# Performance work log

Hardware: AMD Instinct MI355X
Metric: run time of the kernel (lower is better)

## Reference

```python
import jax, jax.numpy as jnp
import numpy as np

B, D_IN, D_H, D_OUT, D_INT = 1024, 2048, 4096, 2048, 1024


def fwht(x):
    """Fast Walsh-Hadamard transform over a length-2^k vector (unnormalized),
    faithful to the torch chunk/cat butterfly loop."""
    n = x.shape[0]
    k = int(n).bit_length() - 1
    for i in range(k):
        y = x.reshape(2 ** i, 2, -1)        # split butterfly level i
        x = jnp.stack([y[:, 0] + y[:, 1], y[:, 0] - y[:, 1]], axis=1)
    return x.reshape(n)


def fastfood(V, BB, Pi, GG, DD):
    """fastfood_torched: pad -> B*x -> H -> permute -> G* -> H -> slice/scale."""
    LL = BB.shape[0]
    vpad = jnp.zeros((LL,), V.dtype).at[: V.shape[0]].set(V)
    m5 = fwht(fwht(BB * vpad)[Pi] * GG)
    divisor = jnp.sqrt(LL * jnp.sum(GG * GG))
    return m5[:DD] / (divisor * np.sqrt(float(DD) / LL))


def _ff_vars(key, DD):
    LL = 1 << int(np.ceil(np.log2(DD)))
    k1, k2, k3 = jax.random.split(key, 3)
    BB = jnp.where(jax.random.uniform(k1, (LL,)) < 0.5, -1.0, 1.0).astype(jnp.float32)
    Pi = jax.random.permutation(k2, LL).astype(jnp.int32)
    GG = jax.random.normal(k3, (LL,), dtype=jnp.float32)
    return BB, Pi, GG


def setup_inputs():
    key = jax.random.key(0)
    ks = jax.random.split(key, 8)
    x = jax.random.normal(ks[0], (B, D_IN), dtype=jnp.float32)
    V = jax.random.normal(ks[1], (D_INT,), dtype=jnp.float32) * 0.01
    W1_0 = jax.random.normal(ks[2], (D_H, D_IN), dtype=jnp.float32) * 0.02
    b1_0 = jnp.zeros((D_H,), jnp.float32)
    W2_0 = jax.random.normal(ks[3], (D_OUT, D_H), dtype=jnp.float32) * 0.02
    b2_0 = jnp.zeros((D_OUT,), jnp.float32)
    BB_W1, Pi_W1, GG_W1 = _ff_vars(ks[4], D_H * D_IN)
    BB_b1, Pi_b1, GG_b1 = _ff_vars(ks[5], D_H)
    BB_W2, Pi_W2, GG_W2 = _ff_vars(ks[6], D_OUT * D_H)
    BB_b2, Pi_b2, GG_b2 = _ff_vars(ks[7], D_OUT)
    return dict(x=x, V=V, W1_0=W1_0, b1_0=b1_0, W2_0=W2_0, b2_0=b2_0,
                BB_W1=BB_W1, Pi_W1=Pi_W1, GG_W1=GG_W1,
                BB_b1=BB_b1, Pi_b1=Pi_b1, GG_b1=GG_b1,
                BB_W2=BB_W2, Pi_W2=Pi_W2, GG_W2=GG_W2,
                BB_b2=BB_b2, Pi_b2=Pi_b2, GG_b2=GG_b2)


def reference(x, V, W1_0, b1_0, W2_0, b2_0,
              BB_W1, Pi_W1, GG_W1, BB_b1, Pi_b1, GG_b1,
              BB_W2, Pi_W2, GG_W2, BB_b2, Pi_b2, GG_b2):
    # Reconstruct each parameter: theta = theta0 + fastfood(V).view(shape)
    W1 = W1_0 + fastfood(V, BB_W1, Pi_W1, GG_W1, D_H * D_IN).reshape(D_H, D_IN)
    b1 = b1_0 + fastfood(V, BB_b1, Pi_b1, GG_b1, D_H)
    W2 = W2_0 + fastfood(V, BB_W2, Pi_W2, GG_W2, D_OUT * D_H).reshape(D_OUT, D_H)
    b2 = b2_0 + fastfood(V, BB_b2, Pi_b2, GG_b2, D_OUT)
    # Wrapped module forward (2-layer MLP)
    h = jax.nn.relu(x @ W1.T + b1)
    return h @ W2.T + b2
```

## Files before the change

### kernel.cpp

```cpp
#include <hip/hip_runtime.h>
#include <hip/hip_bf16.h>
#include <stdint.h>


typedef __attribute__((ext_vector_type(8))) short bf16x8;
typedef __attribute__((ext_vector_type(8))) short short8;
typedef __attribute__((ext_vector_type(4))) float f32x4;

__device__ __forceinline__ ushort f2bf(float f) {
  union { float f; uint32_t u; } v; v.f = f;
  return (ushort)((v.u + 0x7FFFu + ((v.u >> 16) & 1u)) >> 16);
}
__device__ __forceinline__ float bf2f(ushort u) {
  union { uint32_t u; float f; } v; v.u = (uint32_t)u << 16; return v.f;
}

__device__ __forceinline__ void gload_lds16(const void* g, void* l) {
  __builtin_amdgcn_global_load_lds(
      (const __attribute__((address_space(1))) void*)g,
      (__attribute__((address_space(3))) void*)l, 16, 0, 0);
}

__device__ __forceinline__ void wait_vm0()  { asm volatile("s_waitcnt vmcnt(0)"  ::: "memory"); }
__device__ __forceinline__ void wait_lgkm0(){ asm volatile("s_waitcnt lgkmcnt(0)" ::: "memory"); }
__device__ __forceinline__ void barrier_raw(){ asm volatile("s_barrier" ::: "memory"); }
__device__ __forceinline__ void lds_barrier() {
  wait_lgkm0();
  barrier_raw();
  __builtin_amdgcn_sched_barrier(0);
}

template <int NN>
__device__ __forceinline__ void wht_inreg(float* v) {
#pragma unroll
  for (int h = 1; h < NN; h <<= 1)
#pragma unroll
    for (int g = 0; g < NN; g += (h << 1))
#pragma unroll
      for (int k = 0; k < h; ++k) {
        float a = v[g + k], b = v[g + k + h];
        v[g + k] = a + b; v[g + k + h] = a - b;
      }
}

__global__ __launch_bounds__(256) void prep(
    const float4* __restrict__ x4, ushort4* __restrict__ xb4,
    const float* __restrict__ V,
    const float* __restrict__ BBW1, const float* __restrict__ BBW2,
    float* __restrict__ t1, float* __restrict__ t2,
    const float* __restrict__ BBb1, const int* __restrict__ Pib1,
    const float* __restrict__ GGb1, const float* __restrict__ b10,
    const float* __restrict__ BBb2, const int* __restrict__ Pib2,
    const float* __restrict__ GGb2, const float* __restrict__ b20,
    float* __restrict__ ob1, float* __restrict__ ob2) {
  __shared__ float ts[1024];
  __shared__ float zs[4096];
  __shared__ float red[4];
  const int bid = blockIdx.x;
  const int tid = threadIdx.x;

  if (bid < 2048) {
    int i = bid * 256 + tid;
    float4 v = x4[i];
    ushort4 o;
    o.x = f2bf(v.x); o.y = f2bf(v.y); o.z = f2bf(v.z); o.w = f2bf(v.w);
    xb4[i] = o;
    return;
  }

  if (bid < 2050) {
    const int which = bid - 2048;
    const float* BB = which ? BBW2 : BBW1;
    float* t = which ? t2 : t1;
    for (int i = tid; i < 1024; i += 256) ts[i] = BB[i] * V[i];
    for (int st = 0; st < 10; ++st) {
      int half = 1 << st;
      __syncthreads();
      for (int j = tid; j < 512; j += 256) {
        int p = ((j >> st) << (st + 1)) | (j & (half - 1));
        float a = ts[p], b = ts[p + half];
        ts[p] = a + b; ts[p + half] = a - b;
      }
    }
    __syncthreads();
    for (int i = tid; i < 1024; i += 256) t[i] = ts[i];
    return;
  }

  {
    const int which = bid - 2050;
    const int L = which ? 2048 : 4096;
    const float* BB = which ? BBb2 : BBb1;
    const int* Pi = which ? Pib2 : Pib1;
    const float* GG = which ? GGb2 : GGb1;
    const float* b0 = which ? b20 : b10;
    float* ob = which ? ob2 : ob1;

    for (int i = tid; i < 1024; i += 256) ts[i] = BB[i] * V[i];
    for (int st = 0; st < 10; ++st) {
      int half = 1 << st;
      __syncthreads();
      for (int j = tid; j < 512; j += 256) {
        int p = ((j >> st) << (st + 1)) | (j & (half - 1));
        float a = ts[p], b = ts[p + half];
        ts[p] = a + b; ts[p + half] = a - b;
      }
    }
    __syncthreads();
    float gsum = 0.f;
    for (int i = tid; i < L; i += 256) {
      int pi = Pi[i];
      float g = GG[i];
      gsum += g * g;
      zs[i] = ts[pi & 1023] * g;
    }
    for (int o = 32; o > 0; o >>= 1) gsum += __shfl_down(gsum, o);
    if ((tid & 63) == 0) red[tid >> 6] = gsum;
    __syncthreads();
    float ssum = red[0] + red[1] + red[2] + red[3];
    for (int st = 0; (1 << st) < L; ++st) {
      int half = 1 << st;
      __syncthreads();
      for (int j = tid; j < (L >> 1); j += 256) {
        int p = ((j >> st) << (st + 1)) | (j & (half - 1));
        float a = zs[p], b = zs[p + half];
        zs[p] = a + b; zs[p + half] = a - b;
      }
    }
    __syncthreads();
    float scale = rsqrtf((float)L * ssum);
    for (int i = tid; i < L; i += 256) ob[i] = b0[i] + zs[i] * scale;
  }
}

__global__ __launch_bounds__(256) void ff_pass1(
    const int* __restrict__ Pi1, const float* __restrict__ GG1,
    const int* __restrict__ Pi2, const float* __restrict__ GG2,
    const float* __restrict__ t1, const float* __restrict__ t2,
    ushort* __restrict__ inter1, ushort* __restrict__ inter2,
    float* __restrict__ partials) {
  __shared__ float ts[1024];
  __shared__ float zs[8448];
  __shared__ float red[4];
  int tid = threadIdx.x;
  int wsel = blockIdx.x >> 10;
  int blk = blockIdx.x & 1023;
  const int* Pi = wsel ? Pi2 : Pi1;
  const float* GG = wsel ? GG2 : GG1;
  const float* t = wsel ? t2 : t1;
  ushort* inter = wsel ? inter2 : inter1;
  size_t base = (size_t)blk * 8192;

  for (int i = tid; i < 1024; i += 256) ts[i] = t[i];
  __syncthreads();

  const int4* Pi4 = (const int4*)(Pi + base);
  const float4* GG4 = (const float4*)(GG + base);
  float gsum = 0.f;
#pragma unroll
  for (int q = 0; q < 8; ++q) {
    int u = (q << 8) + tid;
    int4 p4 = Pi4[u];
    float4 g4 = GG4[u];
    gsum += g4.x * g4.x + g4.y * g4.y + g4.z * g4.z + g4.w * g4.w;
    int i0 = u << 2;
    float4 z;
    z.x = ts[p4.x & 1023] * g4.x;
    z.y = ts[p4.y & 1023] * g4.y;
    z.z = ts[p4.z & 1023] * g4.z;
    z.w = ts[p4.w & 1023] * g4.w;
    *(float4*)&zs[i0 + (i0 >> 5)] = z;
  }
  for (int o = 32; o > 0; o >>= 1) gsum += __shfl_down(gsum, o);
  if ((tid & 63) == 0) red[tid >> 6] = gsum;
  __syncthreads();
  if (tid == 0) partials[blockIdx.x] = red[0] + red[1] + red[2] + red[3];

  float v[32];
  {
    int o = (tid & 7) | ((tid >> 3) << 8);
#pragma unroll
    for (int r = 0; r < 32; ++r) { int i = o + (r << 3); v[r] = zs[i + (i >> 5)]; }
    wht_inreg<32>(v);
#pragma unroll
    for (int r = 0; r < 32; ++r) { int i = o + (r << 3); zs[i + (i >> 5)] = v[r]; }
  }
  __syncthreads();
  {
#pragma unroll
    for (int r = 0; r < 32; ++r) { int i = tid | (r << 8); v[r] = zs[i + (i >> 5)]; }
    wht_inreg<32>(v);
#pragma unroll
    for (int r = 0; r < 32; ++r) { int i = tid | (r << 8); zs[i + (i >> 5)] = v[r]; }
  }
  __syncthreads();
  {
    int tp = ((tid & 63) << 3) | ((tid >> 6) << 11);
#pragma unroll
    for (int j = 0; j < 4; ++j)
#pragma unroll
      for (int k = 0; k < 8; ++k) { int i = tp + (j << 9) + k; v[(j << 3) + k] = zs[i + (i >> 5)]; }
#pragma unroll
    for (int j = 0; j < 4; ++j) wht_inreg<8>(v + (j << 3));
#pragma unroll
    for (int j = 0; j < 4; ++j) {
      short8 s;
#pragma unroll
      for (int k = 0; k < 8; ++k) s[k] = (short)f2bf(v[(j << 3) + k]);
      *(short8*)(inter + base + tp + (j << 9)) = s;
    }
  }
}

__global__ __launch_bounds__(512) void ff_pass2(
    const ushort* __restrict__ inter1, const ushort* __restrict__ inter2,
    const float* __restrict__ W01, const float* __restrict__ W02,
    const float* __restrict__ partials,
    ushort* __restrict__ W1b, ushort* __restrict__ W2b) {
  __shared__ ushort tile[65536];
  __shared__ float red[8];
  const int tid = threadIdx.x;
  const int wsel = blockIdx.x >> 7;
  const int cb = (blockIdx.x & 127) << 6;
  const ushort* __restrict__ inter = wsel ? inter2 : inter1;
  const float* __restrict__ W0 = wsel ? W02 : W01;
  ushort* __restrict__ Wb = wsel ? W2b : W1b;
  char* tb = (char*)tile;

  float s = partials[(wsel << 10) + tid] + partials[(wsel << 10) + tid + 512];
  for (int o = 32; o > 0; o >>= 1) s += __shfl_down(s, o);
  if ((tid & 63) == 0) red[tid >> 6] = s;

#pragma unroll
  for (int h = 0; h < 2; ++h) {
    int r = tid + (h << 9);
    const ushort* gp = inter + ((size_t)r << 13) + cb;
#pragma unroll
    for (int j = 0; j < 8; ++j) {
      short8 d = *(const short8*)(gp + (j << 3));
      *(short8*)(tb + (r << 7) + ((j ^ (r & 7)) << 4)) = d;
    }
  }
  float4 w0a0[8], w0b0[8];
  {
    const size_t gb = ((size_t)tid << 13) + cb;
#pragma unroll
    for (int j = 0; j < 8; ++j) {
      w0a0[j] = *(const float4*)(W0 + gb + (j << 3));
      w0b0[j] = *(const float4*)(W0 + gb + (j << 3) + 4);
    }
  }
  lds_barrier();
  float ssum = 0.f;
#pragma unroll
  for (int k = 0; k < 8; ++k) ssum += red[k];
  const float sc = rsqrtf(8388608.f * ssum);

  const int p = tid & 31;
  const int j0 = p >> 2;
  const int ob = (p & 3) << 2;
#pragma unroll
  for (int swp = 0; swp < 2; ++swp) {
    const int ge = (tid >> 5) + (swp << 4);
    float va[32], vb[32];
#pragma unroll
    for (int r = 0; r < 32; ++r) {
      int row = (ge << 5) + r;
      ushort2 u = *(const ushort2*)(tb + (row << 7) + ((j0 ^ (row & 7)) << 4) + ob);
      va[r] = bf2f(u.x); vb[r] = bf2f(u.y);
    }
    wht_inreg<32>(va); wht_inreg<32>(vb);
#pragma unroll
    for (int r = 0; r < 32; ++r) {
      int row = (ge << 5) + r;
      ushort2 u; u.x = f2bf(va[r]); u.y = f2bf(vb[r]);
      *(ushort2*)(tb + (row << 7) + ((j0 ^ (row & 7)) << 4) + ob) = u;
    }
  }
  lds_barrier();
#pragma unroll
  for (int swp = 0; swp < 2; ++swp) {
    const int ge = (tid >> 5) + (swp << 4);
    float va[32], vb[32];
#pragma unroll
    for (int r = 0; r < 32; ++r) {
      int row = ge + (r << 5);
      ushort2 u = *(const ushort2*)(tb + (row << 7) + ((j0 ^ (row & 7)) << 4) + ob);
      va[r] = bf2f(u.x); vb[r] = bf2f(u.y);
    }
    wht_inreg<32>(va); wht_inreg<32>(vb);
#pragma unroll
    for (int r = 0; r < 32; ++r) {
      int row = ge + (r << 5);
      ushort2 u; u.x = f2bf(va[r]); u.y = f2bf(vb[r]);
      *(ushort2*)(tb + (row << 7) + ((j0 ^ (row & 7)) << 4) + ob) = u;
    }
  }
  float4 w0a1[8], w0b1[8];
  {
    const size_t gb = ((size_t)(tid + 512) << 13) + cb;
#pragma unroll
    for (int j = 0; j < 8; ++j) {
      w0a1[j] = *(const float4*)(W0 + gb + (j << 3));
      w0b1[j] = *(const float4*)(W0 + gb + (j << 3) + 4);
    }
  }
  lds_barrier();
  {
    const int r = tid;
    const size_t gb = ((size_t)r << 13) + cb;
#pragma unroll
    for (int j = 0; j < 8; ++j) {
      short8 d = *(const short8*)(tb + (r << 7) + ((j ^ (r & 7)) << 4));
      short8 o;
      o[0] = (short)f2bf(bf2f((ushort)d[0]) * sc + w0a0[j].x);
      o[1] = (short)f2bf(bf2f((ushort)d[1]) * sc + w0a0[j].y);
      o[2] = (short)f2bf(bf2f((ushort)d[2]) * sc + w0a0[j].z);
      o[3] = (short)f2bf(bf2f((ushort)d[3]) * sc + w0a0[j].w);
      o[4] = (short)f2bf(bf2f((ushort)d[4]) * sc + w0b0[j].x);
      o[5] = (short)f2bf(bf2f((ushort)d[5]) * sc + w0b0[j].y);
      o[6] = (short)f2bf(bf2f((ushort)d[6]) * sc + w0b0[j].z);
      o[7] = (short)f2bf(bf2f((ushort)d[7]) * sc + w0b0[j].w);
      *(short8*)(Wb + gb + (j << 3)) = o;
    }
  }
  {
    const int r = tid + 512;
    const size_t gb = ((size_t)r << 13) + cb;
#pragma unroll
    for (int j = 0; j < 8; ++j) {
      short8 d = *(const short8*)(tb + (r << 7) + ((j ^ (r & 7)) << 4));
      short8 o;
      o[0] = (short)f2bf(bf2f((ushort)d[0]) * sc + w0a1[j].x);
      o[1] = (short)f2bf(bf2f((ushort)d[1]) * sc + w0a1[j].y);
      o[2] = (short)f2bf(bf2f((ushort)d[2]) * sc + w0a1[j].z);
      o[3] = (short)f2bf(bf2f((ushort)d[3]) * sc + w0a1[j].w);
      o[4] = (short)f2bf(bf2f((ushort)d[4]) * sc + w0b1[j].x);
      o[5] = (short)f2bf(bf2f((ushort)d[5]) * sc + w0b1[j].y);
      o[6] = (short)f2bf(bf2f((ushort)d[6]) * sc + w0b1[j].z);
      o[7] = (short)f2bf(bf2f((ushort)d[7]) * sc + w0b1[j].w);
      *(short8*)(Wb + gb + (j << 3)) = o;
    }
  }
}

template <int NT>
__global__ __launch_bounds__(256) void gemm_sp(
    const ushort* __restrict__ A, const ushort* __restrict__ B,
    ushort* __restrict__ P0, ushort* __restrict__ P1,
    ushort* __restrict__ P2, ushort* __restrict__ P3,
    int M, int N, int K) {
  __shared__ ushort As[2][8192];
  __shared__ ushort Bs[2][8192];
  const int tid = threadIdx.x;
  const int w = tid >> 6, l = tid & 63;
  const int wr = w >> 1, wc = w & 1;
  const int brow = blockIdx.y << 7, bcol = blockIdx.x << 7;
  const int lrow = l >> 3;
  const int csrc = ((l & 7) ^ lrow) << 3;
  const int l15 = l & 15;
  const int x7 = l15 & 7;
  const int z = blockIdx.z;
  const int kb = z * (NT << 6);
  ushort* __restrict__ P = z == 0 ? P0 : z == 1 ? P1 : z == 2 ? P2 : P3;
  f32x4 acc[4][4] = {};

  const ushort* pa = A + (size_t)(brow + (w << 5) + lrow) * K + kb + csrc;
  const ushort* pb = B + (size_t)(bcol + (w << 5) + lrow) * K + kb + csrc;
  const size_t K8 = (size_t)K << 3;

#define STAGE(buf, tt)                                                      \
  {                                                                         \
    const ushort* qa = pa + ((tt) << 6);                                    \
    const ushort* qb = pb + ((tt) << 6);                                    \
    _Pragma("unroll")                                                       \
    for (int i = 0; i < 4; ++i) {                                           \
      gload_lds16(qa + K8 * i, &As[buf][(((w << 2) + i) << 9)]);            \
      gload_lds16(qb + K8 * i, &Bs[buf][(((w << 2) + i) << 9)]);            \
    }                                                                       \
  }

  STAGE(0, 0);
  for (int t = 0; t < NT; ++t) {
    wait_vm0();
    barrier_raw();
    if (t + 1 < NT) STAGE((t + 1) & 1, t + 1);
    const ushort* Acur = As[t & 1];
    const ushort* Bcur = Bs[t & 1];
    bf16x8 af[2][4], bfr[2][4];
#pragma unroll
    for (int kk = 0; kk < 2; ++kk) {
      int c8 = (kk << 2) + (l >> 4);
#pragma unroll
      for (int m = 0; m < 4; ++m)
        af[kk][m] = *(const bf16x8*)&Acur[(((wr << 6) + (m << 4) + l15) << 6) + ((c8 ^ x7) << 3)];
#pragma unroll
      for (int n = 0; n < 4; ++n)
        bfr[kk][n] = *(const bf16x8*)&Bcur[(((wc << 6) + (n << 4) + l15) << 6) + ((c8 ^ x7) << 3)];
    }
    wait_lgkm0();
#pragma unroll
    for (int kk = 0; kk < 2; ++kk)
#pragma unroll
      for (int m = 0; m < 4; ++m)
#pragma unroll
        for (int n = 0; n < 4; ++n)
          acc[m][n] = __builtin_amdgcn_mfma_f32_16x16x32_bf16(af[kk][m], bfr[kk][n], acc[m][n], 0, 0, 0);
  }
#undef STAGE

#pragma unroll
  for (int n = 0; n < 4; ++n) {
    int col = bcol + (wc << 6) + (n << 4) + l15;
#pragma unroll
    for (int m = 0; m < 4; ++m) {
      int row0 = brow + (wr << 6) + (m << 4) + ((l >> 4) << 2);
#pragma unroll
      for (int j = 0; j < 4; ++j)
        P[(size_t)(row0 + j) * N + col] = f2bf(acc[m][n][j]);
    }
  }
}

__global__ __launch_bounds__(256) void hfuse(
    const ushort4* __restrict__ G0, const ushort4* __restrict__ G1,
    const float* __restrict__ b1, ushort4* __restrict__ hb) {
  int i = blockIdx.x * 256 + threadIdx.x;
  ushort4 a = G0[i], b = G1[i];
  const float4 bv = *(const float4*)(b1 + ((i & 1023) << 2));
  ushort4 o;
  o.x = f2bf(fmaxf(bf2f(a.x) + bf2f(b.x) + bv.x, 0.f));
  o.y = f2bf(fmaxf(bf2f(a.y) + bf2f(b.y) + bv.y, 0.f));
  o.z = f2bf(fmaxf(bf2f(a.z) + bf2f(b.z) + bv.z, 0.f));
  o.w = f2bf(fmaxf(bf2f(a.w) + bf2f(b.w) + bv.w, 0.f));
  hb[i] = o;
}

__global__ __launch_bounds__(256) void reduce_out4(
    const ushort4* __restrict__ Q0, const ushort4* __restrict__ Q1,
    const ushort4* __restrict__ Q2, const ushort4* __restrict__ Q3,
    const float* __restrict__ b2, float4* __restrict__ out) {
  int i = blockIdx.x * 256 + threadIdx.x;
  ushort4 a = Q0[i], b = Q1[i], c = Q2[i], d = Q3[i];
  const float4 bb = *(const float4*)(b2 + ((i & 511) << 2));
  float4 o;
  o.x = bf2f(a.x) + bf2f(b.x) + bf2f(c.x) + bf2f(d.x) + bb.x;
  o.y = bf2f(a.y) + bf2f(b.y) + bf2f(c.y) + bf2f(d.y) + bb.y;
  o.z = bf2f(a.z) + bf2f(b.z) + bf2f(c.z) + bf2f(d.z) + bb.z;
  o.w = bf2f(a.w) + bf2f(b.w) + bf2f(c.w) + bf2f(d.w) + bb.w;
  out[i] = o;
}

extern "C" void kernel_launch(void* const* d_in, const int* in_sizes, int n_in,
                              void* d_out, int out_size, void* d_ws, size_t ws_size,
                              hipStream_t stream) {
  const float* x     = (const float*)d_in[0];
  const float* V     = (const float*)d_in[1];
  const float* W1_0  = (const float*)d_in[2];
  const float* b1_0  = (const float*)d_in[3];
  const float* W2_0  = (const float*)d_in[4];
  const float* b2_0  = (const float*)d_in[5];
  const float* BB_W1 = (const float*)d_in[6];
  const int*   Pi_W1 = (const int*)d_in[7];
  const float* GG_W1 = (const float*)d_in[8];
  const float* BB_b1 = (const float*)d_in[9];
  const int*   Pi_b1 = (const int*)d_in[10];
  const float* GG_b1 = (const float*)d_in[11];
  const float* BB_W2 = (const float*)d_in[12];
  const int*   Pi_W2 = (const int*)d_in[13];
  const float* GG_W2 = (const float*)d_in[14];
  const float* BB_b2 = (const float*)d_in[15];
  const int*   Pi_b2 = (const int*)d_in[16];
  const float* GG_b2 = (const float*)d_in[17];
  float* out = (float*)d_out;

  const size_t MB = 1048576ull;
  char* ws = (char*)d_ws;
  ushort* inter1 = (ushort*)(ws);
  ushort* G0     = (ushort*)(ws);
  ushort* G1     = (ushort*)(ws + 8 * MB);
  ushort* inter2 = (ushort*)(ws + 16 * MB);
  ushort* Q0     = (ushort*)(ws + 16 * MB);
  ushort* Q1     = (ushort*)(ws + 20 * MB);
  ushort* Q2     = (ushort*)(ws + 24 * MB);
  ushort* Q3     = (ushort*)(ws + 28 * MB);
  ushort* W1b    = (ushort*)(ws + 32 * MB);
  ushort* W2b    = (ushort*)(ws + 48 * MB);
  ushort* xb     = (ushort*)(ws + 64 * MB);
  ushort* hb     = (ushort*)(ws + 68 * MB);
  char*   S      = ws + 76 * MB;
  float*  t1     = (float*)(S);
  float*  t2     = (float*)(S + 4096);
  float*  b1     = (float*)(S + 8192);
  float*  b2     = (float*)(S + 8192 + 16384);
  float*  parts  = (float*)(S + 8192 + 16384 + 8192);

  prep<<<2052, 256, 0, stream>>>((const float4*)x, (ushort4*)xb, V,
                                 BB_W1, BB_W2, t1, t2,
                                 BB_b1, Pi_b1, GG_b1, b1_0,
                                 BB_b2, Pi_b2, GG_b2, b2_0, b1, b2);

  ff_pass1<<<2048, 256, 0, stream>>>(Pi_W1, GG_W1, Pi_W2, GG_W2, t1, t2,
                                     inter1, inter2, parts);
  ff_pass2<<<256, 512, 0, stream>>>(inter1, inter2, W1_0, W2_0, parts, W1b, W2b);

  gemm_sp<16><<<dim3(32, 8, 2), 256, 0, stream>>>(xb, W1b, G0, G1, nullptr, nullptr,
                                                  1024, 4096, 2048);
  hfuse<<<4096, 256, 0, stream>>>((const ushort4*)G0, (const ushort4*)G1, b1,
                                  (ushort4*)hb);
  gemm_sp<16><<<dim3(16, 8, 4), 256, 0, stream>>>(hb, W2b, Q0, Q1, Q2, Q3,
                                                  1024, 2048, 4096);
  reduce_out4<<<2048, 256, 0, stream>>>((const ushort4*)Q0, (const ushort4*)Q1,
                                        (const ushort4*)Q2, (const ushort4*)Q3,
                                        b2, (float4*)out);
}
```

Baseline: 155.5 us.

## Use 4-stage K=32 LDS pipeline in split-K GEMM instead of double buffering

The split-K bf16 GEMM now stages K tiles of 32 instead of 64 and keeps four LDS buffers, issuing three tiles ahead. It waits with partial vmcnt counts so later loads stay in flight. The swizzle and staging layout are reworked for 32-wide rows, and NT doubles to keep the same K per split. This aims to hide global load latency better, at the cost of twice as many barriers per K and less MFMA work between them.

Result: slower. 161.5 us (+3.9%).

```diff
diff --git a/kernel.cpp b/kernel.cpp
--- a/kernel.cpp
+++ b/kernel.cpp
@@ -21,6 +21,8 @@
       (__attribute__((address_space(3))) void*)l, 16, 0, 0);
 }
 
+__device__ __forceinline__ void wait_vm8()  { asm volatile("s_waitcnt vmcnt(8)"  ::: "memory"); }
+__device__ __forceinline__ void wait_vm4()  { asm volatile("s_waitcnt vmcnt(4)"  ::: "memory"); }
 __device__ __forceinline__ void wait_vm0()  { asm volatile("s_waitcnt vmcnt(0)"  ::: "memory"); }
 __device__ __forceinline__ void wait_lgkm0(){ asm volatile("s_waitcnt lgkmcnt(0)" ::: "memory"); }
 __device__ __forceinline__ void barrier_raw(){ asm volatile("s_barrier" ::: "memory"); }
@@ -350,62 +352,63 @@
     ushort* __restrict__ P0, ushort* __restrict__ P1,
     ushort* __restrict__ P2, ushort* __restrict__ P3,
     int M, int N, int K) {
-  __shared__ ushort As[2][8192];
-  __shared__ ushort Bs[2][8192];
+  __shared__ ushort As[4][4096];
+  __shared__ ushort Bs[4][4096];
   const int tid = threadIdx.x;
   const int w = tid >> 6, l = tid & 63;
   const int wr = w >> 1, wc = w & 1;
   const int brow = blockIdx.y << 7, bcol = blockIdx.x << 7;
-  const int lrow = l >> 3;
-  const int csrc = ((l & 7) ^ lrow) << 3;
+  const int srow = tid >> 2;
+  const int sg = tid & 3;
+  const int csrc = (sg ^ ((srow >> 1) & 3)) << 3;
   const int l15 = l & 15;
-  const int x7 = l15 & 7;
+  const int c8 = l >> 4;
+  const int gx = (l15 >> 1) & 3;
   const int z = blockIdx.z;
-  const int kb = z * (NT << 6);
+  const int kb = z * (NT << 5);
   ushort* __restrict__ P = z == 0 ? P0 : z == 1 ? P1 : z == 2 ? P2 : P3;
   f32x4 acc[4][4] = {};
 
-  const ushort* pa = A + (size_t)(brow + (w << 5) + lrow) * K + kb + csrc;
-  const ushort* pb = B + (size_t)(bcol + (w << 5) + lrow) * K + kb + csrc;
-  const size_t K8 = (size_t)K << 3;
-
-#define STAGE(buf, tt)                                                      \
-  {                                                                         \
-    const ushort* qa = pa + ((tt) << 6);                                    \
-    const ushort* qb = pb + ((tt) << 6);                                    \
-    _Pragma("unroll")                                                       \
-    for (int i = 0; i < 4; ++i) {                                           \
-      gload_lds16(qa + K8 * i, &As[buf][(((w << 2) + i) << 9)]);            \
-      gload_lds16(qb + K8 * i, &Bs[buf][(((w << 2) + i) << 9)]);            \
-    }                                                                       \
-  }
-
-  STAGE(0, 0);
+  const ushort* pa = A + (size_t)(brow + srow) * K + kb + csrc;
+  const ushort* pb = B + (size_t)(bcol + srow) * K + kb + csrc;
+  const size_t K64 = (size_t)K << 6;
+
+#define STAGE(buf, tt)                                                \
+  {                                                                   \
+    const ushort* qa = pa + ((tt) << 5);                              \
+    const ushort* qb = pb + ((tt) << 5);                              \
+    gload_lds16(qa,       (char*)As[buf] + (tid << 4));               \
+    gload_lds16(qa + K64, (char*)As[buf] + 4096 + (tid << 4));        \
+    gload_lds16(qb,       (char*)Bs[buf] + (tid << 4));               \
+    gload_lds16(qb + K64, (char*)Bs[buf] + 4096 + (tid << 4));        \
+  }
+
+  STAGE(0, 0); STAGE(1, 1); STAGE(2, 2);
   for (int t = 0; t < NT; ++t) {
-    wait_vm0();
+    if (t < NT - 2) wait_vm8();
+    else if (t == NT - 2) wait_vm4();
+    else wait_vm0();
     barrier_raw();
-    if (t + 1 < NT) STAGE((t + 1) & 1, t + 1);
-    const ushort* Acur = As[t & 1];
-    const ushort* Bcur = Bs[t & 1];
-    bf16x8 af[2][4], bfr[2][4];
-#pragma unroll
-    for (int kk = 0; kk < 2; ++kk) {
-      int c8 = (kk << 2) + (l >> 4);
-#pragma unroll
-      for (int m = 0; m < 4; ++m)
-        af[kk][m] = *(const bf16x8*)&Acur[(((wr << 6) + (m << 4) + l15) << 6) + ((c8 ^ x7) << 3)];
+    if (t + 3 < NT) STAGE((t + 3) & 3, t + 3);
+    const ushort* Acur = As[t & 3];
+    const ushort* Bcur = Bs[t & 3];
+    bf16x8 af[4], bfr[4];
+#pragma unroll
+    for (int m = 0; m < 4; ++m) {
+      int ra = (wr << 6) + (m << 4) + l15;
+      af[m] = *(const bf16x8*)&Acur[(ra << 5) + ((c8 ^ gx) << 3)];
+    }
+#pragma unroll
+    for (int n = 0; n < 4; ++n) {
+      int rb = (wc << 6) + (n << 4) + l15;
+      bfr[n] = *(const bf16x8*)&Bcur[(rb << 5) + ((c8 ^ gx) << 3)];
+    }
+    wait_lgkm0();
+#pragma unroll
+    for (int m = 0; m < 4; ++m)
 #pragma unroll
       for (int n = 0; n < 4; ++n)
-        bfr[kk][n] = *(const bf16x8*)&Bcur[(((wc << 6) + (n << 4) + l15) << 6) + ((c8 ^ x7) << 3)];
-    }
-    wait_lgkm0();
-#pragma unroll
-    for (int kk = 0; kk < 2; ++kk)
-#pragma unroll
-      for (int m = 0; m < 4; ++m)
-#pragma unroll
-        for (int n = 0; n < 4; ++n)
-          acc[m][n] = __builtin_amdgcn_mfma_f32_16x16x32_bf16(af[kk][m], bfr[kk][n], acc[m][n], 0, 0, 0);
+        acc[m][n] = __builtin_amdgcn_mfma_f32_16x16x32_bf16(af[m], bfr[n], acc[m][n], 0, 0, 0);
   }
 #undef STAGE
 
@@ -504,11 +507,11 @@
                                      inter1, inter2, parts);
   ff_pass2<<<256, 512, 0, stream>>>(inter1, inter2, W1_0, W2_0, parts, W1b, W2b);
 
-  gemm_sp<16><<<dim3(32, 8, 2), 256, 0, stream>>>(xb, W1b, G0, G1, nullptr, nullptr,
+  gemm_sp<32><<<dim3(32, 8, 2), 256, 0, stream>>>(xb, W1b, G0, G1, nullptr, nullptr,
                                                   1024, 4096, 2048);
   hfuse<<<4096, 256, 0, stream>>>((const ushort4*)G0, (const ushort4*)G1, b1,
                                   (ushort4*)hb);
-  gemm_sp<16><<<dim3(16, 8, 4), 256, 0, stream>>>(hb, W2b, Q0, Q1, Q2, Q3,
+  gemm_sp<32><<<dim3(16, 8, 4), 256, 0, stream>>>(hb, W2b, Q0, Q1, Q2, Q3,
                                                   1024, 2048, 4096);
   reduce_out4<<<2048, 256, 0, stream>>>((const ushort4*)Q0, (const ushort4*)Q1,
                                         (const ushort4*)Q2, (const ushort4*)Q3,
```
